# Performance work log

Hardware: AMD Instinct MI355X
Metric: run time of the kernel (lower is better)

Reference implementation:

```python
import jax, jax.numpy as jnp
import numpy as np

B, C, H, W = 4, 2048, 32, 32
HID, A, G = 512, 9, 20
SCALE = 32.0
POS_T, NEG_T = 0.7, 0.3
W_CONF, W_REG = 1.0, 5.0
EPS = 1e-8


def _anchor_base():
    # gen_anc_centers + gen_anc_base: centers at (i+0.5); anc_w=scale, anc_h=scale*ratio; clipped to feature-map extent
    scales = jnp.array([2.0, 4.0, 6.0])
    ratios = jnp.array([0.5, 1.0, 1.5])
    aw = jnp.repeat(scales, 3)                       # [A]
    ah = (scales[:, None] * ratios[None, :]).reshape(-1)
    xc = (jnp.arange(W) + 0.5)[None, :, None]        # [1,W,1]
    yc = (jnp.arange(H) + 0.5)[:, None, None]        # [H,1,1]
    x1 = jnp.clip(xc - aw / 2, 0.0, W)
    y1 = jnp.clip(yc - ah / 2, 0.0, H)
    x2 = jnp.clip(xc + aw / 2, 0.0, W)
    y2 = jnp.clip(yc + ah / 2, 0.0, H)
    anc = jnp.stack(jnp.broadcast_arrays(x1, y1, x2, y2), axis=-1)  # [H,W,A,4]
    return anc.reshape(-1, 4)                        # [N,4], N = H*W*A


def _conv(x, w, b):
    y = jax.lax.conv_general_dilated(x, w, (1, 1), 'SAME',
                                     dimension_numbers=('NCHW', 'OIHW', 'NCHW'))
    return y + b[None, :, None, None]


def setup_inputs():
    key = jax.random.key(0)
    ks = jax.random.split(key, 8)
    feature_map = jax.random.normal(ks[0], (B, C, H, W), jnp.float32)
    # valid GT boxes in pixel coords of a 1024x1024 image
    ctr = jax.random.uniform(ks[1], (B, G, 2), minval=0.15, maxval=0.85) * 1024.0
    wh = jax.random.uniform(ks[2], (B, G, 2), minval=0.05, maxval=0.30) * 1024.0
    gt_bboxes = jnp.clip(jnp.concatenate([ctr - wh / 2, ctr + wh / 2], -1), 0.0, 1024.0)
    gt_classes = jax.random.randint(ks[3], (B, G), 1, 21)
    f1 = 1.0 / np.sqrt(C * 9)
    f2 = 1.0 / np.sqrt(HID)
    conv1_w = jax.random.uniform(ks[4], (HID, C, 3, 3), jnp.float32, -f1, f1)
    conv1_b = jnp.zeros((HID,), jnp.float32)
    conf_w = jax.random.uniform(ks[5], (A, HID, 1, 1), jnp.float32, -f2, f2)
    conf_b = jnp.zeros((A,), jnp.float32)
    reg_w = jax.random.uniform(ks[6], (A * 4, HID, 1, 1), jnp.float32, -f2, f2)
    reg_b = jnp.zeros((A * 4,), jnp.float32)
    return {"feature_map": feature_map, "gt_bboxes": gt_bboxes, "gt_classes": gt_classes,
            "conv1_w": conv1_w, "conv1_b": conv1_b, "conf_w": conf_w, "conf_b": conf_b,
            "reg_w": reg_w, "reg_b": reg_b}


def reference(feature_map, gt_bboxes, gt_classes, conv1_w, conv1_b, conf_w, conf_b, reg_w, reg_b):
    # ProposalModule (dropout = eval identity)
    hid = jax.nn.relu(_conv(feature_map, conv1_w, conv1_b))
    conf = _conv(hid, conf_w, conf_b).transpose(0, 2, 3, 1).reshape(B, -1)       # [B,N]
    offs = _conv(hid, reg_w, reg_b).transpose(0, 2, 3, 1).reshape(B, -1, 4)      # [B,N,4]

    anc = _anchor_base()                              # [N,4]
    gt = gt_bboxes / SCALE                            # project_bboxes p2a

    # IoU [B,N,G]
    lt = jnp.maximum(anc[None, :, None, :2], gt[:, None, :, :2])
    rb = jnp.minimum(anc[None, :, None, 2:], gt[:, None, :, 2:])
    inter = jnp.clip(rb - lt, 0.0).prod(-1)
    area_a = (anc[:, 2] - anc[:, 0]) * (anc[:, 3] - anc[:, 1])
    area_g = (gt[..., 2] - gt[..., 0]) * (gt[..., 3] - gt[..., 1])
    iou = inter / (area_a[None, :, None] + area_g[:, None, :] - inter + EPS)

    # positive: IoU > pos_thresh OR best anchor for each GT; negative: max IoU < neg_thresh
    max_per_gt = iou.max(axis=1, keepdims=True)
    pos = ((iou > POS_T) | ((iou == max_per_gt) & (max_per_gt > EPS))).any(-1)    # [B,N]
    max_per_anc = iou.max(-1)
    gi = iou.argmax(-1)                               # assigned GT per anchor
    neg = (max_per_anc < NEG_T) & (~pos)

    assigned = jnp.take_along_axis(gt, jnp.broadcast_to(gi[:, :, None], gi.shape + (4,)), axis=1)

    acx = (anc[:, 0] + anc[:, 2]) / 2; acy = (anc[:, 1] + anc[:, 3]) / 2
    aw_ = anc[:, 2] - anc[:, 0];       ah_ = anc[:, 3] - anc[:, 1]
    gcx = (assigned[..., 0] + assigned[..., 2]) / 2; gcy = (assigned[..., 1] + assigned[..., 3]) / 2
    gw = assigned[..., 2] - assigned[..., 0];        gh = assigned[..., 3] - assigned[..., 1]
    gt_off = jnp.stack([(gcx - acx) / (aw_ + EPS), (gcy - acy) / (ah_ + EPS),
                        jnp.log((gw + EPS) / (aw_ + EPS)), jnp.log((gh + EPS) / (ah_ + EPS))], -1)

    posf = pos.astype(conf.dtype)
    negf = neg.astype(conf.dtype)
    # BCE-with-logits, reduction='sum' / batch_size (pos target 1, neg target 0)
    cls_loss = ((jax.nn.softplus(-conf) * posf).sum() + (jax.nn.softplus(conf) * negf).sum()) / B
    d = offs - gt_off
    sl1 = jnp.where(jnp.abs(d) < 1.0, 0.5 * d * d, jnp.abs(d) - 0.5)
    reg_loss = (sl1 * posf[..., None]).sum() / B
    total = W_CONF * cls_loss + W_REG * reg_loss

    # generate_proposals from positive anchors + predicted offsets (mask instead of gather for jit)
    pcx = acx + offs[..., 0] * aw_; pcy = acy + offs[..., 1] * ah_
    pw = aw_ * jnp.exp(offs[..., 2]); ph = ah_ * jnp.exp(offs[..., 3])
    proposals = jnp.stack([pcx - pw / 2, pcy - ph / 2, pcx + pw / 2, pcy + ph / 2], -1)
    proposals = proposals * posf[..., None]
    return total, proposals, pos
```

## Files before the change

### kernel.cpp

```cpp
#include <hip/hip_runtime.h>


typedef __bf16 bf16x8 __attribute__((ext_vector_type(8)));
typedef float floatx4 __attribute__((ext_vector_type(4)));

#define NB 4
#define NC 2048
#define NH 32
#define NW 32
#define NHID 512
#define NA 9
#define NG 20
#define NANC 9216
#define NM 4096

#define OFF_XH    0ull
#define OFF_WT    18939904ull
#define OFF_WH    37814272ull
#define OFF_HB    37863424ull
#define OFF_MAXG  37863680ull
#define OFF_SUMS  37864192ull
#define OFF_CTR   37864320ull
#define OFF_HIDP  37864448ull

#define PREP_TX   4096
#define PREP_W    1024
#define PREP_WH   96
#define PREP_HALO 528
#define PREP_MAXG 80
#define PREP_NBLK (PREP_TX + PREP_W + PREP_WH + PREP_HALO + PREP_MAXG + 1)

__device__ __forceinline__ unsigned short f2bf(float f) {
  unsigned int u = __float_as_uint(f);
  u = (u + 0x7fffu + ((u >> 16) & 1u)) >> 16;
  return (unsigned short)u;
}

__device__ __forceinline__ void gload16(const void* g, void* l) {
  __builtin_amdgcn_global_load_lds(
      (const __attribute__((address_space(1))) unsigned int*)g,
      (__attribute__((address_space(3))) unsigned int*)l, 16, 0, 0);
}

__constant__ float c_aw[9] = {2.f,2.f,2.f,4.f,4.f,4.f,6.f,6.f,6.f};
__constant__ float c_ah[9] = {1.f,2.f,3.f,2.f,4.f,6.f,3.f,6.f,9.f};
__constant__ int c_dsp[9] = {-71680, -69632, -67584, -2048, 0, 2048, 67584, 69632, 71680};

struct Anc { float x1, y1, x2, y2, areaA; };
__device__ __forceinline__ Anc anc_of(int n) {
  const int a = n % 9, pix = n / 9;
  const int xi = pix & 31, yi = pix >> 5;
  const float hw = c_aw[a]*0.5f, hh = c_ah[a]*0.5f;
  const float xc = xi + 0.5f, yc = yi + 0.5f;
  Anc A;
  A.x1 = fminf(fmaxf(xc - hw, 0.f), 32.f);
  A.y1 = fminf(fmaxf(yc - hh, 0.f), 32.f);
  A.x2 = fminf(fmaxf(xc + hw, 0.f), 32.f);
  A.y2 = fminf(fmaxf(yc + hh, 0.f), 32.f);
  A.areaA = __fmul_rn(__fsub_rn(A.x2, A.x1), __fsub_rn(A.y2, A.y1));
  return A;
}
__device__ __forceinline__ float iou_one(const Anc& A, float4 gp) {
  const float gx1 = gp.x * 0.03125f, gy1 = gp.y * 0.03125f;
  const float gx2 = gp.z * 0.03125f, gy2 = gp.w * 0.03125f;
  const float dx = fmaxf(__fsub_rn(fminf(A.x2, gx2), fmaxf(A.x1, gx1)), 0.f);
  const float dy = fmaxf(__fsub_rn(fminf(A.y2, gy2), fmaxf(A.y1, gy1)), 0.f);
  const float inter = __fmul_rn(dx, dy);
  const float areaG = __fmul_rn(__fsub_rn(gx2, gx1), __fsub_rn(gy2, gy1));
  const float den = __fadd_rn(__fsub_rn(__fadd_rn(A.areaA, areaG), inter), 1e-8f);
  return __fdiv_rn(inter, den);
}

__global__ __launch_bounds__(256) void k_prep(const float* __restrict__ x,
                                              const float* __restrict__ w1,
                                              const float* __restrict__ cw, const float* __restrict__ cb,
                                              const float* __restrict__ rw, const float* __restrict__ rb,
                                              const float* __restrict__ gtb,
                                              unsigned short* __restrict__ xh,
                                              unsigned short* __restrict__ wt,
                                              unsigned short* __restrict__ wh, float* __restrict__ hb,
                                              unsigned int* __restrict__ maxg,
                                              float* __restrict__ sums, unsigned int* __restrict__ ctr) {
  __shared__ float tile[64][33];
  __shared__ unsigned short wlds[9*1024];
  __shared__ float red[4];
  const int bid = blockIdx.x;
  const int tid = threadIdx.x;

  if (bid < PREP_TX) {
    const int c0 = (bid & 31) << 6;
    const int h  = (bid >> 5) & 31;
    const int b  = bid >> 10;
    const int w = tid & 31, cl = tid >> 5;
    const float* src = x + (((size_t)b*NC + c0)*NH + h)*NW;
#pragma unroll
    for (int j = 0; j < 8; ++j) {
      const int c = cl + j*8;
      tile[c][w] = src[(size_t)c*NH*NW + w];
    }
    __syncthreads();
    unsigned short* dst = xh + ((size_t)(b*34 + h + 1)*34 + 1)*2048 + c0;
    const int w2 = tid >> 3, c8 = (tid & 7) << 3;
    unsigned int pk[4];
#pragma unroll
    for (int k = 0; k < 4; ++k) {
      const unsigned int lo = f2bf(tile[c8 + 2*k][w2]);
      const unsigned int hi = f2bf(tile[c8 + 2*k + 1][w2]);
      pk[k] = lo | (hi << 16);
    }
    *(uint4*)(dst + (size_t)w2*2048 + c8) = make_uint4(pk[0], pk[1], pk[2], pk[3]);
    return;
  }
  if (bid < PREP_TX + PREP_W) {
    const int p = bid - PREP_TX;
    const int o = p >> 1, half = p & 1;
    const int c_base = half << 10;
    const float* src = w1 + ((size_t)(o*2048 + c_base))*9;
#pragma unroll
    for (int j = 0; j < 9; ++j) {
      const int f0 = (j*256 + tid)*4;
      const float4 v = *(const float4*)(src + f0);
      const float vv[4] = {v.x, v.y, v.z, v.w};
#pragma unroll
      for (int e = 0; e < 4; ++e) {
        const int f = f0 + e;
        const int c = f/9, g = f - c*9;
        wlds[g*1024 + c] = f2bf(vv[e]);
      }
    }
    __syncthreads();
#pragma unroll
    for (int j = 0; j < 5; ++j) {
      const int idx = j*256 + tid;
      if (idx < 1152) {
        const int g = idx >> 7, off = (idx & 127) << 3;
        *(uint4*)(wt + (size_t)g*NHID*NC + o*2048 + c_base + off) =
            *(const uint4*)(wlds + g*1024 + off);
      }
    }
    return;
  }
  if (bid < PREP_TX + PREP_W + PREP_WH) {
    const int t = (bid - PREP_TX - PREP_W)*256 + tid;
    const int n = t >> 9, c = t & 511;
    float v = 0.f;
    if (n < 9) v = cw[n*512 + c];
    else if (n < 45) v = rw[(n-9)*512 + c];
    wh[t] = f2bf(v);
    if (c == 0) {
      float bv = 0.f;
      if (n < 9) bv = cb[n];
      else if (n < 45) bv = rb[n-9];
      hb[n] = bv;
    }
    return;
  }
  if (bid < PREP_TX + PREP_W + PREP_WH + PREP_HALO) {
    const int q = bid - (PREP_TX + PREP_W + PREP_WH);
    const int b = q / 132, hc = q - b*132;
    int hh, ww;
    if (hc < 34)       { hh = 0;        ww = hc; }
    else if (hc < 68)  { hh = 33;       ww = hc - 34; }
    else if (hc < 100) { hh = hc - 67;  ww = 0; }
    else               { hh = hc - 99;  ww = 33; }
    uint4* dst = (uint4*)(xh + ((size_t)((b*34 + hh)*34 + ww))*2048);
    dst[tid] = make_uint4(0u, 0u, 0u, 0u);
    return;
  }
  if (bid < PREP_TX + PREP_W + PREP_WH + PREP_HALO + PREP_MAXG) {
    const int p = bid - (PREP_TX + PREP_W + PREP_WH + PREP_HALO);
    const int b = p / NG, g = p - b*NG;
    const float4 gp = *(const float4*)(gtb + ((size_t)b*NG + g)*4);
    float m = 0.f;
#pragma unroll
    for (int j = 0; j < 36; ++j)
      m = fmaxf(m, iou_one(anc_of(tid + j*256), gp));
#pragma unroll
    for (int o = 32; o > 0; o >>= 1) m = fmaxf(m, __shfl_xor(m, o));
    if ((tid & 63) == 0) red[tid >> 6] = m;
    __syncthreads();
    if (tid == 0)
      maxg[b*NG + g] = __float_as_uint(fmaxf(fmaxf(red[0], red[1]), fmaxf(red[2], red[3])));
    return;
  }
  if (tid < 2) sums[tid] = 0.f;
  else if (tid == 2) *ctr = 0u;
}

__device__ __forceinline__ void wgbar() {
  asm volatile("" ::: "memory");
  __builtin_amdgcn_s_barrier();
  asm volatile("" ::: "memory");
}

__global__ __launch_bounds__(512) void k_conv_gemm(const unsigned short* __restrict__ xh,
                                                   const unsigned short* __restrict__ wt,
                                                   unsigned short* __restrict__ hidp,
                                                   int csplit, int ksh) {
  __shared__ unsigned short As[2][256*64] __attribute__((aligned(16)));
  __shared__ unsigned short Bs[2][256*64] __attribute__((aligned(16)));
  const int t = threadIdx.x;
  const int L = blockIdx.x;
  const int kz = L & ((1 << ksh) - 1);
  const int tile = L >> ksh;
  const int tileM = tile & 15, tileN = tile >> 4;
  const int o0 = tileN << 8;
  const int wv = t >> 6, lane = t & 63;
  const int wm = wv >> 2, wn = wv & 3;
  const int quad = lane >> 4, l16 = lane & 15;
  const int c_base = kz * csplit;
  const int tpg = csplit >> 6;
  const int NT = 9 * tpg;

  floatx4 acc[8][4];
#pragma unroll
  for (int mt = 0; mt < 8; ++mt)
#pragma unroll
    for (int nt = 0; nt < 4; ++nt)
      acc[mt][nt] = (floatx4){0.f, 0.f, 0.f, 0.f};

  const int lr = lane >> 3, pos = lane & 7;
  int gA[4], gB[4];
#pragma unroll
  for (int j = 0; j < 4; ++j) {
    const int r = j*64 + wv*8 + lr;
    const int sd = (pos - r) & 7;
    const int pix = tileM*256 + r;
    const int b = pix >> 10;
    const int hh = ((pix >> 5) & 31) + 1, ww = (pix & 31) + 1;
    gA[j] = ((b*34 + hh)*34 + ww)*2048 + c_base + sd*8;
    gB[j] = (o0 + r)*2048 + c_base + sd*8;
  }

  {
    const int dsp = c_dsp[0];
#pragma unroll
    for (int j = 0; j < 4; ++j)
      gload16(xh + gA[j] + dsp, &As[0][(j*64 + wv*8)*64]);
#pragma unroll
    for (int j = 0; j < 4; ++j)
      gload16(wt + gB[j], &Bs[0][(j*64 + wv*8)*64]);
  }

  int gq = 0, cq = 0, buf = 0;
  for (int kt = 0; kt < NT; ++kt) {
    int ng = gq, ncq = cq + 1;
    if (ncq == tpg) { ncq = 0; ++ng; }
    if (kt + 1 < NT) {
      const int dsp = c_dsp[ng], co = ncq << 6;
      const size_t wgo = (size_t)ng * NHID * NC;
#pragma unroll
      for (int j = 0; j < 4; ++j)
        gload16(xh + gA[j] + dsp + co, &As[buf^1][(j*64 + wv*8)*64]);
#pragma unroll
      for (int j = 0; j < 4; ++j)
        gload16(wt + wgo + gB[j] + co, &Bs[buf^1][(j*64 + wv*8)*64]);
      asm volatile("s_waitcnt vmcnt(8)" ::: "memory");
    } else {
      asm volatile("s_waitcnt vmcnt(0)" ::: "memory");
    }
    wgbar();

    const unsigned short* Asb = As[buf];
    const unsigned short* Bsb = Bs[buf];
#pragma unroll
    for (int sub = 0; sub < 2; ++sub) {
      const int ps = ((sub*4 + quad) + l16) & 7;
      bf16x8 af[8], bw[4];
#pragma unroll
      for (int mt = 0; mt < 8; ++mt)
        af[mt] = *(const bf16x8*)(Asb + (wm*128 + mt*16 + l16)*64 + ps*8);
#pragma unroll
      for (int nt = 0; nt < 4; ++nt)
        bw[nt] = *(const bf16x8*)(Bsb + (wn*64 + nt*16 + l16)*64 + ps*8);
#pragma unroll
      for (int mt = 0; mt < 8; ++mt)
#pragma unroll
        for (int nt = 0; nt < 4; ++nt)
          acc[mt][nt] = __builtin_amdgcn_mfma_f32_16x16x32_bf16(af[mt], bw[nt], acc[mt][nt], 0, 0, 0);
    }
    wgbar();
    gq = ng; cq = ncq; buf ^= 1;
  }

  unsigned short* hp = hidp + (size_t)kz*NM*NHID;
  const int m0 = tileM*256 + wm*128;
  const int oc = o0 + wn*64;
#pragma unroll
  for (int mt = 0; mt < 8; ++mt) {
    const int m = m0 + mt*16 + quad*4;
#pragma unroll
    for (int nt = 0; nt < 4; ++nt) {
      const int o = oc + nt*16 + l16;
#pragma unroll
      for (int r = 0; r < 4; ++r)
        hp[(size_t)(m + r)*NHID + o] = f2bf(acc[mt][nt][r]);
    }
  }
}

__device__ __forceinline__ float softplusf(float z) {
  return fmaxf(z, 0.f) + log1pf(expf(-fabsf(z)));
}
__device__ __forceinline__ float sl1f(float d) {
  const float ad = fabsf(d);
  return ad < 1.f ? 0.5f*d*d : ad - 0.5f;
}

__global__ __launch_bounds__(256) void k_heads_assign(const unsigned short* __restrict__ hidp,
                                                      const float* __restrict__ b1,
                                                      const unsigned short* __restrict__ wh,
                                                      const float* __restrict__ hb,
                                                      const float* __restrict__ gtb,
                                                      const unsigned int* __restrict__ maxg,
                                                      float* __restrict__ out,
                                                      float* __restrict__ sums,
                                                      unsigned int* __restrict__ ctr,
                                                      int nsplit) {
  __shared__ float red[4][16][48];
  __shared__ float hl[16][49];
  __shared__ float4 gt_s[20];
  __shared__ float  mg_s[20];
  const int t = threadIdx.x;
  const int bid = blockIdx.x;
  const int b = bid >> 6, pix0 = (bid & 63) << 4;

  if (t < 20) {
    gt_s[t] = *(const float4*)(gtb + ((size_t)b*NG + t)*4);
    mg_s[t] = __uint_as_float(maxg[b*NG + t]);
  }

  const int wv = t >> 6, lane = t & 63;
  const int quad = lane >> 4, l16 = lane & 15;
  floatx4 acc[3];
#pragma unroll
  for (int nt = 0; nt < 3; ++nt) acc[nt] = (floatx4){0.f, 0.f, 0.f, 0.f};

  const int m = bid*16 + l16;
#pragma unroll
  for (int kk = 0; kk < 4; ++kk) {
    const int ch0 = wv*128 + kk*32 + quad*8;
    float s[8] = {0.f,0.f,0.f,0.f,0.f,0.f,0.f,0.f};
    const size_t gi = (size_t)m*NHID + ch0;
    for (int sp = 0; sp < nsplit; ++sp) {
      const uint4 v = *(const uint4*)(hidp + (size_t)sp*NM*NHID + gi);
      s[0] += __uint_as_float(v.x << 16); s[1] += __uint_as_float(v.x & 0xffff0000u);
      s[2] += __uint_as_float(v.y << 16); s[3] += __uint_as_float(v.y & 0xffff0000u);
      s[4] += __uint_as_float(v.z << 16); s[5] += __uint_as_float(v.z & 0xffff0000u);
      s[6] += __uint_as_float(v.w << 16); s[7] += __uint_as_float(v.w & 0xffff0000u);
    }
    union { unsigned short u[8]; bf16x8 v; } af;
#pragma unroll
    for (int e = 0; e < 8; ++e)
      af.u[e] = f2bf(fmaxf(s[e] + b1[ch0 + e], 0.f));
#pragma unroll
    for (int nt = 0; nt < 3; ++nt) {
      const bf16x8 bf = *(const bf16x8*)(wh + (size_t)(nt*16 + l16)*NHID + ch0);
      acc[nt] = __builtin_amdgcn_mfma_f32_16x16x32_bf16(af.v, bf, acc[nt], 0, 0, 0);
    }
  }
#pragma unroll
  for (int nt = 0; nt < 3; ++nt)
#pragma unroll
    for (int r = 0; r < 4; ++r)
      red[wv][quad*4 + r][nt*16 + l16] = acc[nt][r];
  __syncthreads();
#pragma unroll
  for (int j = 0; j < 3; ++j) {
    const int idx = t + j*256;
    const int i = idx / 48, c = idx - i*48;
    hl[i][c] = red[0][i][c] + red[1][i][c] + red[2][i][c] + red[3][i][c] + hb[c];
  }
  __syncthreads();

  float cs = 0.f, rs = 0.f;
  if (t < 144) {
    const int pixL = t / 9, a = t - pixL*9;
    const int pix = pix0 + pixL;
    const int n = pix*9 + a;
    const int idx = b*NANC + n;
    const Anc A = anc_of(n);

    float mx = -1.f; int gi = 0; bool pos = false;
    for (int g = 0; g < NG; ++g) {
      const float v = iou_one(A, gt_s[g]);
      const float mg = mg_s[g];
      pos = pos || (v > 0.7f) || ((v == mg) && (mg > 1e-8f));
      if (v > mx) { mx = v; gi = g; }
    }
    const bool neg = (mx < 0.3f) && !pos;
    const float posf = pos ? 1.f : 0.f;

    const float conf = hl[pixL][a];
    const float of0 = hl[pixL][9 + a*4 + 0];
    const float of1 = hl[pixL][9 + a*4 + 1];
    const float of2 = hl[pixL][9 + a*4 + 2];
    const float of3 = hl[pixL][9 + a*4 + 3];

    if (pos) cs = softplusf(-conf);
    else if (neg) cs = softplusf(conf);

    const float acx = (A.x1 + A.x2)*0.5f, acy = (A.y1 + A.y2)*0.5f;
    const float aw = A.x2 - A.x1, ah = A.y2 - A.y1;
    if (pos) {
      const float4 gp = gt_s[gi];
      const float gx1 = gp.x*0.03125f, gy1 = gp.y*0.03125f;
      const float gx2 = gp.z*0.03125f, gy2 = gp.w*0.03125f;
      const float gcx = (gx1+gx2)*0.5f, gcy = (gy1+gy2)*0.5f;
      const float gw = gx2-gx1, gh = gy2-gy1;
      const float t0 = (gcx-acx)/(aw+1e-8f), t1 = (gcy-acy)/(ah+1e-8f);
      const float t2 = logf((gw+1e-8f)/(aw+1e-8f)), t3 = logf((gh+1e-8f)/(ah+1e-8f));
      rs = sl1f(of0-t0) + sl1f(of1-t1) + sl1f(of2-t2) + sl1f(of3-t3);
    }

    const float pcx = acx + of0*aw, pcy = acy + of1*ah;
    const float pw = aw*expf(of2), ph = ah*expf(of3);
    float* op = out + 1 + (size_t)idx*4;
    op[0] = (pcx - pw*0.5f)*posf;
    op[1] = (pcy - ph*0.5f)*posf;
    op[2] = (pcx + pw*0.5f)*posf;
    op[3] = (pcy + ph*0.5f)*posf;
    out[1 + 4*(size_t)NB*NANC + idx] = posf;
  }
#pragma unroll
  for (int o = 32; o > 0; o >>= 1) { cs += __shfl_xor(cs, o); rs += __shfl_xor(rs, o); }
  if ((t & 63) == 0) { atomicAdd(&sums[0], cs); atomicAdd(&sums[1], rs); }

  __syncthreads();
  if (t == 0) {
    __threadfence();
    const unsigned int c = atomicAdd(ctr, 1u);
    if (c == 255u) {
      __threadfence();
      const float fcs = atomicAdd(&sums[0], 0.f);
      const float frs = atomicAdd(&sums[1], 0.f);
      out[0] = fcs*0.25f + 5.f*(frs*0.25f);
    }
  }
}

extern "C" void kernel_launch(void* const* d_in, const int* in_sizes, int n_in,
                              void* d_out, int out_size, void* d_ws, size_t ws_size,
                              hipStream_t stream) {
  const float* x   = (const float*)d_in[0];
  const float* gtb = (const float*)d_in[1];
  const float* w1  = (const float*)d_in[3];
  const float* b1  = (const float*)d_in[4];
  const float* cw  = (const float*)d_in[5];
  const float* cb  = (const float*)d_in[6];
  const float* rw  = (const float*)d_in[7];
  const float* rb  = (const float*)d_in[8];
  float* out = (float*)d_out;
  char* ws = (char*)d_ws;

  unsigned short* xh    = (unsigned short*)(ws + OFF_XH);
  unsigned short* wt    = (unsigned short*)(ws + OFF_WT);
  unsigned short* wh    = (unsigned short*)(ws + OFF_WH);
  float*          hb    = (float*)(ws + OFF_HB);
  unsigned int*   maxg  = (unsigned int*)(ws + OFF_MAXG);
  float*          sums  = (float*)(ws + OFF_SUMS);
  unsigned int*   ctr   = (unsigned int*)(ws + OFF_CTR);
  unsigned short* hidp  = (unsigned short*)(ws + OFF_HIDP);

  int nsplit = 8, ksh = 3;
  while (nsplit > 1 && OFF_HIDP + (size_t)nsplit*NM*NHID*2 > ws_size) { nsplit >>= 1; --ksh; }
  const int csplit = NC / nsplit;

  k_prep<<<PREP_NBLK, 256, 0, stream>>>(x, w1, cw, cb, rw, rb, gtb, xh, wt, wh, hb, maxg, sums, ctr);
  k_conv_gemm<<<32*nsplit, 512, 0, stream>>>(xh, wt, hidp, csplit, ksh);
  k_heads_assign<<<256, 256, 0, stream>>>(hidp, b1, wh, hb, gtb, maxg, out, sums, ctr, nsplit);
}
```

Measured before the change: 231.8 us.

## Restructure conv GEMM main loop into four-phase pipelined schedule with split-K LDS halves

The conv GEMM K-tile is split into two 32-wide halves in LDS, and the loop runs in four phases. Each phase issues one quarter of the next stages' global-to-LDS loads, reads a subset of fragments, and runs 16 MFMAs under raised s_setprio. This is meant to interleave memory traffic with matrix math more finely and to cut register pressure, targeting two workgroups per CU via launch_bounds(512,2). The cost is more barriers per K-tile and more fragile vmcnt bookkeeping. It also assumes tpg is a power of two matching tsh = 5 - ksh.

```diff
diff --git a/kernel.cpp b/kernel.cpp
--- a/kernel.cpp
+++ b/kernel.cpp
@@ -41,6 +41,8 @@
       (const __attribute__((address_space(1))) unsigned int*)g,
       (__attribute__((address_space(3))) unsigned int*)l, 16, 0, 0);
 }
+
+#define VMCNT(n) asm volatile("s_waitcnt vmcnt(" #n ")" ::: "memory")
 
 __constant__ float c_aw[9] = {2.f,2.f,2.f,4.f,4.f,4.f,6.f,6.f,6.f};
 __constant__ float c_ah[9] = {1.f,2.f,3.f,2.f,4.f,6.f,3.f,6.f,9.f};
@@ -193,12 +195,12 @@
   asm volatile("" ::: "memory");
 }
 
-__global__ __launch_bounds__(512) void k_conv_gemm(const unsigned short* __restrict__ xh,
-                                                   const unsigned short* __restrict__ wt,
-                                                   unsigned short* __restrict__ hidp,
-                                                   int csplit, int ksh) {
-  __shared__ unsigned short As[2][256*64] __attribute__((aligned(16)));
-  __shared__ unsigned short Bs[2][256*64] __attribute__((aligned(16)));
+__global__ __launch_bounds__(512, 2) void k_conv_gemm(const unsigned short* __restrict__ xh,
+                                                      const unsigned short* __restrict__ wt,
+                                                      unsigned short* __restrict__ hidp,
+                                                      int csplit, int ksh) {
+  __shared__ unsigned short As[2][2][256*32] __attribute__((aligned(16)));
+  __shared__ unsigned short Bs[2][2][256*32] __attribute__((aligned(16)));
   const int t = threadIdx.x;
   const int L = blockIdx.x;
   const int kz = L & ((1 << ksh) - 1);
@@ -210,6 +212,7 @@
   const int quad = lane >> 4, l16 = lane & 15;
   const int c_base = kz * csplit;
   const int tpg = csplit >> 6;
+  const int tsh = 5 - ksh;
   const int NT = 9 * tpg;
 
   floatx4 acc[8][4];
@@ -219,69 +222,103 @@
     for (int nt = 0; nt < 4; ++nt)
       acc[mt][nt] = (floatx4){0.f, 0.f, 0.f, 0.f};
 
-  const int lr = lane >> 3, pos = lane & 7;
-  int gA[4], gB[4];
-#pragma unroll
-  for (int j = 0; j < 4; ++j) {
-    const int r = j*64 + wv*8 + lr;
-    const int sd = (pos - r) & 7;
+  const int lr4 = lane >> 2;
+  const int sq = ((lane & 3) - lr4) & 3;
+  int gA[2], gB[2];
+#pragma unroll
+  for (int j = 0; j < 2; ++j) {
+    const int r = wv*32 + j*16 + lr4;
     const int pix = tileM*256 + r;
     const int b = pix >> 10;
     const int hh = ((pix >> 5) & 31) + 1, ww = (pix & 31) + 1;
-    gA[j] = ((b*34 + hh)*34 + ww)*2048 + c_base + sd*8;
-    gB[j] = (o0 + r)*2048 + c_base + sd*8;
-  }
-
-  {
-    const int dsp = c_dsp[0];
-#pragma unroll
-    for (int j = 0; j < 4; ++j)
-      gload16(xh + gA[j] + dsp, &As[0][(j*64 + wv*8)*64]);
-#pragma unroll
-    for (int j = 0; j < 4; ++j)
-      gload16(wt + gB[j], &Bs[0][(j*64 + wv*8)*64]);
-  }
-
-  int gq = 0, cq = 0, buf = 0;
+    gA[j] = ((b*34 + hh)*34 + ww)*2048 + c_base + sq*8;
+    gB[j] = (o0 + r)*2048 + c_base + sq*8;
+  }
+  const int ldst0 = (wv*32)*32, ldst1 = (wv*32 + 16)*32;
+
+  auto stage = [&](int tau, int part) {
+    if (tau >= NT) return;
+    const int isB = part & 1, ks = part >> 1;
+    const int sbuf = tau & 1;
+    const int gs = tau >> tsh, cqs = tau & (tpg - 1);
+    const int coff = cqs*64 + ks*32;
+    if (!isB) {
+      const int d = c_dsp[gs] + coff;
+      gload16(xh + gA[0] + d, &As[sbuf][ks][ldst0]);
+      gload16(xh + gA[1] + d, &As[sbuf][ks][ldst1]);
+    } else {
+      const size_t wo = (size_t)gs*NHID*NC + coff;
+      gload16(wt + wo + gB[0], &Bs[sbuf][ks][ldst0]);
+      gload16(wt + wo + gB[1], &Bs[sbuf][ks][ldst1]);
+    }
+  };
+
+  const int ps = ((quad + l16) & 3) * 8;
+  int aoff[8], boff[4];
+#pragma unroll
+  for (int mt = 0; mt < 8; ++mt) aoff[mt] = (wm*128 + mt*16 + l16)*32 + ps;
+#pragma unroll
+  for (int nt = 0; nt < 4; ++nt) boff[nt] = (wn*64 + nt*16 + l16)*32 + ps;
+
+  stage(0, 0); stage(0, 1); stage(0, 2); stage(0, 3);
+  stage(1, 0); stage(1, 1);
+  VMCNT(8);
+  wgbar();
+
+#define MFMA16(MH) do { \
+    __builtin_amdgcn_s_setprio(1); \
+    _Pragma("unroll") \
+    for (int mt = 0; mt < 4; ++mt) \
+      _Pragma("unroll") \
+      for (int nt = 0; nt < 4; ++nt) \
+        acc[(MH)*4 + mt][nt] = __builtin_amdgcn_mfma_f32_16x16x32_bf16(af[mt], bw[nt], acc[(MH)*4 + mt][nt], 0, 0, 0); \
+    __builtin_amdgcn_s_setprio(0); \
+  } while (0)
+
   for (int kt = 0; kt < NT; ++kt) {
-    int ng = gq, ncq = cq + 1;
-    if (ncq == tpg) { ncq = 0; ++ng; }
-    if (kt + 1 < NT) {
-      const int dsp = c_dsp[ng], co = ncq << 6;
-      const size_t wgo = (size_t)ng * NHID * NC;
-#pragma unroll
-      for (int j = 0; j < 4; ++j)
-        gload16(xh + gA[j] + dsp + co, &As[buf^1][(j*64 + wv*8)*64]);
-#pragma unroll
-      for (int j = 0; j < 4; ++j)
-        gload16(wt + wgo + gB[j] + co, &Bs[buf^1][(j*64 + wv*8)*64]);
-      asm volatile("s_waitcnt vmcnt(8)" ::: "memory");
-    } else {
-      asm volatile("s_waitcnt vmcnt(0)" ::: "memory");
-    }
-    wgbar();
-
-    const unsigned short* Asb = As[buf];
-    const unsigned short* Bsb = Bs[buf];
-#pragma unroll
-    for (int sub = 0; sub < 2; ++sub) {
-      const int ps = ((sub*4 + quad) + l16) & 7;
-      bf16x8 af[8], bw[4];
-#pragma unroll
-      for (int mt = 0; mt < 8; ++mt)
-        af[mt] = *(const bf16x8*)(Asb + (wm*128 + mt*16 + l16)*64 + ps*8);
-#pragma unroll
-      for (int nt = 0; nt < 4; ++nt)
-        bw[nt] = *(const bf16x8*)(Bsb + (wn*64 + nt*16 + l16)*64 + ps*8);
-#pragma unroll
-      for (int mt = 0; mt < 8; ++mt)
-#pragma unroll
-        for (int nt = 0; nt < 4; ++nt)
-          acc[mt][nt] = __builtin_amdgcn_mfma_f32_16x16x32_bf16(af[mt], bw[nt], acc[mt][nt], 0, 0, 0);
-    }
-    wgbar();
-    gq = ng; cq = ncq; buf ^= 1;
-  }
+    const int buf = kt & 1;
+    const unsigned short* A0 = &As[buf][0][0];
+    const unsigned short* A1 = &As[buf][1][0];
+    const unsigned short* B0 = &Bs[buf][0][0];
+    const unsigned short* B1 = &Bs[buf][1][0];
+    bf16x8 af[4], bw[4];
+
+#pragma unroll
+    for (int nt = 0; nt < 4; ++nt) bw[nt] = *(const bf16x8*)(B0 + boff[nt]);
+#pragma unroll
+    for (int mt = 0; mt < 4; ++mt) af[mt] = *(const bf16x8*)(A0 + aoff[mt]);
+    stage(kt + 1, 2);
+    wgbar();
+    MFMA16(0);
+    wgbar();
+
+#pragma unroll
+    for (int mt = 0; mt < 4; ++mt) af[mt] = *(const bf16x8*)(A0 + aoff[4 + mt]);
+    stage(kt + 1, 3);
+    if (kt < NT - 1) { VMCNT(8); } else { VMCNT(0); }
+    wgbar();
+    MFMA16(1);
+    wgbar();
+
+#pragma unroll
+    for (int nt = 0; nt < 4; ++nt) bw[nt] = *(const bf16x8*)(B1 + boff[nt]);
+#pragma unroll
+    for (int mt = 0; mt < 4; ++mt) af[mt] = *(const bf16x8*)(A1 + aoff[mt]);
+    stage(kt + 2, 0);
+    wgbar();
+    MFMA16(0);
+    wgbar();
+
+#pragma unroll
+    for (int mt = 0; mt < 4; ++mt) af[mt] = *(const bf16x8*)(A1 + aoff[4 + mt]);
+    stage(kt + 2, 1);
+    if (kt < NT - 2) { VMCNT(8); }
+    else if (kt == NT - 2) { VMCNT(4); }
+    wgbar();
+    MFMA16(1);
+    wgbar();
+  }
+#undef MFMA16
 
   unsigned short* hp = hidp + (size_t)kz*NM*NHID;
   const int m0 = tileM*256 + wm*128;
```

New measurement: 236.9 us. +2.2%, slower.

## Interleave next-tile global loads across four MFMA quarter phases in conv GEMM

Applied to the files above, without the earlier changes.

Splits each K-step of the conv GEMM into four quarter phases. Each phase loads a slice of A fragments from LDS, issues part of the next tile's global-to-LDS copies, waits with staged vmcnt counts, and then runs its MFMAs at raised s_setprio. The aim is to spread memory traffic across the compute and hide load latency better than issuing every prefetch at the top of the loop. It also sets launch_bounds(512,2), which caps registers per thread. With the 128-register accumulator that cap risks spills, and the shared-memory footprint may still prevent two blocks per CU. The extra barriers per K-step add synchronisation overhead.

```diff
diff --git a/kernel.cpp b/kernel.cpp
--- a/kernel.cpp
+++ b/kernel.cpp
@@ -41,6 +41,8 @@
       (const __attribute__((address_space(1))) unsigned int*)g,
       (__attribute__((address_space(3))) unsigned int*)l, 16, 0, 0);
 }
+
+#define VMCNT(n) asm volatile("s_waitcnt vmcnt(" #n ")" ::: "memory")
 
 __constant__ float c_aw[9] = {2.f,2.f,2.f,4.f,4.f,4.f,6.f,6.f,6.f};
 __constant__ float c_ah[9] = {1.f,2.f,3.f,2.f,4.f,6.f,3.f,6.f,9.f};
@@ -193,10 +195,10 @@
   asm volatile("" ::: "memory");
 }
 
-__global__ __launch_bounds__(512) void k_conv_gemm(const unsigned short* __restrict__ xh,
-                                                   const unsigned short* __restrict__ wt,
-                                                   unsigned short* __restrict__ hidp,
-                                                   int csplit, int ksh) {
+__global__ __launch_bounds__(512, 2) void k_conv_gemm(const unsigned short* __restrict__ xh,
+                                                      const unsigned short* __restrict__ wt,
+                                                      unsigned short* __restrict__ hidp,
+                                                      int csplit, int ksh) {
   __shared__ unsigned short As[2][256*64] __attribute__((aligned(16)));
   __shared__ unsigned short Bs[2][256*64] __attribute__((aligned(16)));
   const int t = threadIdx.x;
@@ -210,6 +212,7 @@
   const int quad = lane >> 4, l16 = lane & 15;
   const int c_base = kz * csplit;
   const int tpg = csplit >> 6;
+  const int tsh = 5 - ksh;
   const int NT = 9 * tpg;
 
   floatx4 acc[8][4];
@@ -222,66 +225,104 @@
   const int lr = lane >> 3, pos = lane & 7;
   int gA[4], gB[4];
 #pragma unroll
-  for (int j = 0; j < 4; ++j) {
-    const int r = j*64 + wv*8 + lr;
-    const int sd = (pos - r) & 7;
-    const int pix = tileM*256 + r;
+  for (int u = 0; u < 4; ++u) {
+    const int row = u*64 + wv*8 + lr;
+    const int sd = (pos - row) & 7;
+    const int pix = tileM*256 + row;
     const int b = pix >> 10;
     const int hh = ((pix >> 5) & 31) + 1, ww = (pix & 31) + 1;
-    gA[j] = ((b*34 + hh)*34 + ww)*2048 + c_base + sd*8;
-    gB[j] = (o0 + r)*2048 + c_base + sd*8;
-  }
-
-  {
-    const int dsp = c_dsp[0];
-#pragma unroll
-    for (int j = 0; j < 4; ++j)
-      gload16(xh + gA[j] + dsp, &As[0][(j*64 + wv*8)*64]);
-#pragma unroll
-    for (int j = 0; j < 4; ++j)
-      gload16(wt + gB[j], &Bs[0][(j*64 + wv*8)*64]);
-  }
-
-  int gq = 0, cq = 0, buf = 0;
+    gA[u] = ((b*34 + hh)*34 + ww)*2048 + c_base + sd*8;
+    gB[u] = (o0 + row)*2048 + c_base + sd*8;
+  }
+
+  auto stageA = [&](int tau, int u) {
+    if (tau >= NT) return;
+    const int g = tau >> tsh, cq = tau & (tpg - 1);
+    gload16(xh + gA[u] + c_dsp[g] + cq*64, &As[tau & 1][(u*64 + wv*8)*64]);
+  };
+  auto stageB = [&](int tau, int u) {
+    if (tau >= NT) return;
+    const int g = tau >> tsh, cq = tau & (tpg - 1);
+    gload16(wt + (size_t)g*NHID*NC + cq*64 + gB[u], &Bs[tau & 1][(u*64 + wv*8)*64]);
+  };
+
+  stageB(0, 0); stageB(0, 1); stageB(0, 2); stageB(0, 3);
+  stageA(0, 0); stageA(0, 2);
+  stageA(0, 1); stageA(0, 3);
+  VMCNT(2);
+  wgbar();
+
+#define MFMA_Q(Q) do { \
+    __builtin_amdgcn_s_setprio(1); \
+    _Pragma("unroll") \
+    for (int s = 0; s < 2; ++s) \
+      _Pragma("unroll") \
+      for (int i = 0; i < 2; ++i) \
+        _Pragma("unroll") \
+        for (int nt = 0; nt < 4; ++nt) \
+          acc[2*(Q) + i][nt] = __builtin_amdgcn_mfma_f32_16x16x32_bf16(af[i][s], bw[nt][s], acc[2*(Q) + i][nt], 0, 0, 0); \
+    __builtin_amdgcn_s_setprio(0); \
+  } while (0)
+
   for (int kt = 0; kt < NT; ++kt) {
-    int ng = gq, ncq = cq + 1;
-    if (ncq == tpg) { ncq = 0; ++ng; }
-    if (kt + 1 < NT) {
-      const int dsp = c_dsp[ng], co = ncq << 6;
-      const size_t wgo = (size_t)ng * NHID * NC;
-#pragma unroll
-      for (int j = 0; j < 4; ++j)
-        gload16(xh + gA[j] + dsp + co, &As[buf^1][(j*64 + wv*8)*64]);
-#pragma unroll
-      for (int j = 0; j < 4; ++j)
-        gload16(wt + wgo + gB[j] + co, &Bs[buf^1][(j*64 + wv*8)*64]);
-      asm volatile("s_waitcnt vmcnt(8)" ::: "memory");
-    } else {
-      asm volatile("s_waitcnt vmcnt(0)" ::: "memory");
-    }
-    wgbar();
-
-    const unsigned short* Asb = As[buf];
-    const unsigned short* Bsb = Bs[buf];
-#pragma unroll
-    for (int sub = 0; sub < 2; ++sub) {
-      const int ps = ((sub*4 + quad) + l16) & 7;
-      bf16x8 af[8], bw[4];
-#pragma unroll
-      for (int mt = 0; mt < 8; ++mt)
-        af[mt] = *(const bf16x8*)(Asb + (wm*128 + mt*16 + l16)*64 + ps*8);
+    const int buf = kt & 1;
+    const unsigned short* A = &As[buf][0];
+    const unsigned short* B = &Bs[buf][0];
+    bf16x8 bw[4][2], af[2][2];
+
+#pragma unroll
+    for (int s = 0; s < 2; ++s) {
+      const int ps = ((s*4 + quad) + l16) & 7;
 #pragma unroll
       for (int nt = 0; nt < 4; ++nt)
-        bw[nt] = *(const bf16x8*)(Bsb + (wn*64 + nt*16 + l16)*64 + ps*8);
-#pragma unroll
-      for (int mt = 0; mt < 8; ++mt)
-#pragma unroll
-        for (int nt = 0; nt < 4; ++nt)
-          acc[mt][nt] = __builtin_amdgcn_mfma_f32_16x16x32_bf16(af[mt], bw[nt], acc[mt][nt], 0, 0, 0);
-    }
-    wgbar();
-    gq = ng; cq = ncq; buf ^= 1;
-  }
+        bw[nt][s] = *(const bf16x8*)(B + (wn*64 + nt*16 + l16)*64 + ps*8);
+#pragma unroll
+      for (int i = 0; i < 2; ++i)
+        af[i][s] = *(const bf16x8*)(A + (wm*128 + (0*2 + i)*16 + l16)*64 + ps*8);
+    }
+    stageB(kt + 1, 0); stageB(kt + 1, 1); stageB(kt + 1, 2);
+    wgbar();
+    MFMA_Q(0);
+    wgbar();
+
+#pragma unroll
+    for (int s = 0; s < 2; ++s) {
+      const int ps = ((s*4 + quad) + l16) & 7;
+#pragma unroll
+      for (int i = 0; i < 2; ++i)
+        af[i][s] = *(const bf16x8*)(A + (wm*128 + (1*2 + i)*16 + l16)*64 + ps*8);
+    }
+    stageB(kt + 1, 3); stageA(kt + 1, 0); stageA(kt + 1, 2);
+    if (kt + 1 < NT) { VMCNT(6); } else { VMCNT(0); }
+    wgbar();
+    MFMA_Q(1);
+    wgbar();
+
+#pragma unroll
+    for (int s = 0; s < 2; ++s) {
+      const int ps = ((s*4 + quad) + l16) & 7;
+#pragma unroll
+      for (int i = 0; i < 2; ++i)
+        af[i][s] = *(const bf16x8*)(A + (wm*128 + (2*2 + i)*16 + l16)*64 + ps*8);
+    }
+    stageA(kt + 1, 1); stageA(kt + 1, 3);
+    wgbar();
+    MFMA_Q(2);
+    wgbar();
+
+#pragma unroll
+    for (int s = 0; s < 2; ++s) {
+      const int ps = ((s*4 + quad) + l16) & 7;
+#pragma unroll
+      for (int i = 0; i < 2; ++i)
+        af[i][s] = *(const bf16x8*)(A + (wm*128 + (3*2 + i)*16 + l16)*64 + ps*8);
+    }
+    if (kt + 1 < NT) { VMCNT(2); }
+    wgbar();
+    MFMA_Q(3);
+    wgbar();
+  }
+#undef MFMA_Q
 
   unsigned short* hp = hidp + (size_t)kz*NM*NHID;
   const int m0 = tileM*256 + wm*128;
```

After: 230.7 us. Within noise of the previous version (-0.5%).
